# Kernel optimization log

Measured on AMD Instinct MI355X. Metric: run time of the kernel, lower is better.

## Reference

```python
import jax, jax.numpy as jnp
import numpy as np

N, P, Q, H_DIM, HEADS, D = 4096, 128, 128, 256, 8, 64  # D = graph_dim // heads


def setup_inputs() -> dict:
    key = jax.random.key(0)
    ks = jax.random.split(key, 6)
    s = 0.05  # small scale to keep tanh/softmax in a sane range
    return {
        "x_prices": jax.random.normal(ks[0], (N, P), jnp.float32),
        "x_news": jax.random.normal(ks[1], (N, Q), jnp.float32),
        "W_bil": jax.random.normal(ks[2], (H_DIM, P, Q), jnp.float32) * s,
        "b_bil": jax.random.normal(ks[3], (H_DIM,), jnp.float32) * s,
        "Wt": jax.random.normal(ks[4], (HEADS, D, H_DIM), jnp.float32) * s,
        "a_vec": jax.random.normal(ks[5], (HEADS, 2 * D), jnp.float32) * s,
    }


def reference(x_prices, x_news, W_bil, b_bil, Wt, a_vec):
    # nn.Bilinear: out[n,h] = sum_pq x_prices[n,p] W[h,p,q] x_news[n,q] + b[h]
    x = jnp.einsum('np,hpq,nq->nh', x_prices, W_bil, x_news) + b_bil  # (N, hidden)

    # Per-head linear transform: fc_transform (no bias). Wt: (heads, d, hidden)
    xt = jnp.einsum('nh,kdh->knd', x, Wt)  # (heads, N, d)

    # Attention score a . [x_i, x_j] split into src/dst halves -> broadcast add
    d = Wt.shape[1]
    a_src, a_dst = a_vec[:, :d], a_vec[:, d:]
    s_src = jnp.einsum('knd,kd->kn', xt, a_src)  # (heads, N)
    s_dst = jnp.einsum('knd,kd->kn', xt, a_dst)  # (heads, N)
    scores = s_src[:, :, None] + s_dst[:, None, :]  # (heads, N, N)
    scores = jnp.where(scores >= 0, scores, 0.2 * scores)  # LeakyReLU(0.2)

    attn = jax.nn.softmax(scores, axis=-1)  # softmax over neighbors j
    out = jnp.einsum('knm,kmd->knd', attn, xt)  # (heads, N, d)

    # Concatenate head outputs on feature dim, then tanh
    out = jnp.transpose(out, (1, 0, 2)).reshape(xt.shape[1], -1)  # (N, heads*d)
    return jnp.tanh(out)
```

## Files before the change

kernel.cpp:

```cpp
#include <hip/hip_runtime.h>
#include <hip/hip_bf16.h>

typedef unsigned short ushort;
typedef unsigned int uint;
typedef unsigned long long u64;
typedef _Float16 f16;

#define NN 4096
#define PP 128
#define QQ 128
#define HD 256
#define KH 8
#define DD 64
#define KK 16384

typedef _Float16 f16x2 __attribute__((ext_vector_type(2)));
typedef _Float16 f16x4 __attribute__((ext_vector_type(4)));
typedef _Float16 f16x8 __attribute__((ext_vector_type(8)));
typedef __fp16 fp16x2 __attribute__((ext_vector_type(2)));
typedef float f32x4 __attribute__((ext_vector_type(4)));

__device__ inline void async_lds16(const void* g, void* l) {
  __builtin_amdgcn_global_load_lds(
      (const __attribute__((address_space(1))) unsigned int*)g,
      (__attribute__((address_space(3))) unsigned int*)l, 16, 0, 0);
}

__global__ __launch_bounds__(256) void k0_split2(
    const float* __restrict__ W, const float* __restrict__ Wt,
    f16* __restrict__ hiW, f16* __restrict__ loW,
    f16* __restrict__ hiT, f16* __restrict__ loT, float* __restrict__ xz) {
  const int tid = blockIdx.x * 256 + threadIdx.x;
  const int i = tid * 4;
  if (tid < (NN * HD) / 4)
    *(float4*)&xz[i] = make_float4(0.f, 0.f, 0.f, 0.f);
  const float* src;
  f16 *hi, *lo;
  int off;
  if (i < HD * PP * QQ) { src = W; hi = hiW; lo = loW; off = i; }
  else { src = Wt; hi = hiT; lo = loT; off = i - HD * PP * QQ; }
  const float4 w = *(const float4*)&src[off];
  const float wf[4] = {w.x, w.y, w.z, w.w};
  f16x4 hv, lv;
#pragma unroll
  for (int j = 0; j < 4; ++j) {
    const f16 h = (f16)wf[j];
    hv[j] = h;
    lv[j] = (f16)(wf[j] - (float)h);
  }
  *(f16x4*)&hi[off] = hv;
  *(f16x4*)&lo[off] = lv;
}

__global__ __launch_bounds__(256, 4) void k1_bilinear(
    const float* __restrict__ xp, const float* __restrict__ xn,
    const f16* __restrict__ Whi, const f16* __restrict__ Wlo,
    float* __restrict__ xout) {
  __shared__ f16 whi[128 * 32];
  __shared__ f16 wlo[128 * 32];
  __shared__ f16 zhi[128 * 40];
  __shared__ float xpt[8][128];

  const int t = threadIdx.x;
  const int n0 = blockIdx.x * 128;
  const int kb = blockIdx.y * (KK / 16);
  const int h0 = blockIdx.z * 128;
  const int pb = kb >> 7;

  for (int idx = t; idx < 1024; idx += 256) {
    const int p = idx & 7, n = idx >> 3;
    xpt[p][n] = xp[(size_t)(n0 + n) * PP + pb + p];
  }

  const int l = t & 63, w = t >> 6;
  const int wr = (w >> 1) * 64, wc = (w & 1) * 64;

  int aoff[4], boff[4];
#pragma unroll
  for (int i = 0; i < 4; ++i)
    aoff[i] = (wr + i * 16 + (l & 15)) * 40 + (l >> 4) * 8;
#pragma unroll
  for (int j = 0; j < 4; ++j) {
    const int hr = wc + j * 16 + (l & 15);
    boff[j] = hr * 32 + (((l >> 4) ^ ((hr ^ (hr >> 2)) & 3)) * 8);
  }

  const int shb = t >> 2, seg = t & 3;
  int gsw[2];
#pragma unroll
  for (int g = 0; g < 2; ++g) {
    const int r = shb + 64 * g;
    gsw[g] = seg ^ ((r ^ (r >> 2)) & 3);
  }

  const int zn = t >> 1, zko = (t & 1) * 16;

  f32x4 acc[4][4];
#pragma unroll
  for (int i = 0; i < 4; ++i)
#pragma unroll
    for (int j = 0; j < 4; ++j) acc[i][j] = (f32x4)0.f;

  for (int c = 0; c < 32; ++c) {
    const int kc = kb + c * 32;
    const int pl = c >> 2;
    const int q0 = (c & 3) * 32;

    __syncthreads();

#pragma unroll
    for (int g = 0; g < 2; ++g) {
      const int r = shb + 64 * g;
      async_lds16(Whi + (size_t)(h0 + r) * KK + kc + gsw[g] * 8,
                  whi + r * 32 + seg * 8);
      async_lds16(Wlo + (size_t)(h0 + r) * KK + kc + gsw[g] * 8,
                  wlo + r * 32 + seg * 8);
    }

    {
      const float xpv = xpt[pl][zn];
      const float* xr = xn + (size_t)(n0 + zn) * QQ + q0 + zko;
      const float4 v0 = ((const float4*)xr)[0];
      const float4 v1 = ((const float4*)xr)[1];
      const float4 v2 = ((const float4*)xr)[2];
      const float4 v3 = ((const float4*)xr)[3];
      float zz[16] = {v0.x, v0.y, v0.z, v0.w, v1.x, v1.y, v1.z, v1.w,
                      v2.x, v2.y, v2.z, v2.w, v3.x, v3.y, v3.z, v3.w};
      union { uint u[8]; uint4 q[2]; } ph;
#pragma unroll
      for (int j = 0; j < 8; ++j) {
        union { fp16x2 h; uint u; } cv;
        cv.h = __builtin_amdgcn_cvt_pkrtz(xpv * zz[2 * j], xpv * zz[2 * j + 1]);
        ph.u[j] = cv.u;
      }
      const int zo = zn * 40 + zko;
      *(uint4*)&zhi[zo] = ph.q[0];
      *(uint4*)&zhi[zo + 8] = ph.q[1];
    }

    __syncthreads();

    f16x8 Ah[4];
#pragma unroll
    for (int i = 0; i < 4; ++i) Ah[i] = *(const f16x8*)&zhi[aoff[i]];
#pragma unroll
    for (int j = 0; j < 4; ++j) {
      const f16x8 Bh = *(const f16x8*)&whi[boff[j]];
      const f16x8 Bl = *(const f16x8*)&wlo[boff[j]];
#pragma unroll
      for (int i = 0; i < 4; ++i)
        acc[i][j] = __builtin_amdgcn_mfma_f32_16x16x32_f16(Ah[i], Bh, acc[i][j], 0, 0, 0);
#pragma unroll
      for (int i = 0; i < 4; ++i)
        acc[i][j] = __builtin_amdgcn_mfma_f32_16x16x32_f16(Ah[i], Bl, acc[i][j], 0, 0, 0);
    }
  }

#pragma unroll
  for (int i = 0; i < 4; ++i)
#pragma unroll
    for (int j = 0; j < 4; ++j) {
      const int row = n0 + wr + i * 16 + (l >> 4) * 4;
      const int col = h0 + wc + j * 16 + (l & 15);
#pragma unroll
      for (int r = 0; r < 4; ++r)
        atomicAdd(&xout[(size_t)(row + r) * HD + col], acc[i][j][r]);
    }
}

__global__ __launch_bounds__(256) void k23_xt(
    const float* __restrict__ x, const float* __restrict__ bb,
    const f16* __restrict__ Wthi, const f16* __restrict__ Wtlo,
    const float* __restrict__ av, float* __restrict__ xt,
    float* __restrict__ ssrc, float* __restrict__ sdst) {
  __shared__ f16 ah[64 * 40];
  __shared__ f16 bh[128 * 32];
  __shared__ f16 bl[128 * 32];
  __shared__ float red1[2][64][17];
  __shared__ float red2[2][64][17];
  const int t = threadIdx.x;
  const int n0 = blockIdx.x * 64;
  const int c0 = blockIdx.y * 128;
  const int l = t & 63, w = t >> 6;
  const int wn = (w & 1) * 32, wcc = (w >> 1) * 64;

  int aoff[2], boff[4];
#pragma unroll
  for (int i = 0; i < 2; ++i)
    aoff[i] = (wn + i * 16 + (l & 15)) * 40 + (l >> 4) * 8;
#pragma unroll
  for (int j = 0; j < 4; ++j) {
    const int hr = wcc + j * 16 + (l & 15);
    boff[j] = hr * 32 + (((l >> 4) ^ ((hr ^ (hr >> 2)) & 3)) * 8);
  }

  f32x4 acc[2][4];
#pragma unroll
  for (int i = 0; i < 2; ++i)
#pragma unroll
    for (int j = 0; j < 4; ++j) acc[i][j] = (f32x4)0.f;

  for (int kc = 0; kc < HD; kc += 32) {
    __syncthreads();
    {
      const int row = t >> 2, sg = t & 3;
      const float* xr = &x[(size_t)(n0 + row) * HD + kc + sg * 8];
      const float4 xa = ((const float4*)xr)[0];
      const float4 xb = ((const float4*)xr)[1];
      const float4 ba = *(const float4*)&bb[kc + sg * 8];
      const float4 bv = *(const float4*)&bb[kc + sg * 8 + 4];
      f16x8 o;
      o[0] = (f16)(xa.x + ba.x); o[1] = (f16)(xa.y + ba.y);
      o[2] = (f16)(xa.z + ba.z); o[3] = (f16)(xa.w + ba.w);
      o[4] = (f16)(xb.x + bv.x); o[5] = (f16)(xb.y + bv.y);
      o[6] = (f16)(xb.z + bv.z); o[7] = (f16)(xb.w + bv.w);
      *(f16x8*)&ah[row * 40 + sg * 8] = o;
    }
#pragma unroll
    for (int g = 0; g < 2; ++g) {
      const int slot = g * 256 + t;
      const int col = slot >> 2, ps = slot & 3;
      const int ls = ps ^ ((col ^ (col >> 2)) & 3);
      *(uint4*)&bh[col * 32 + ps * 8] =
          *(const uint4*)&Wthi[(size_t)(c0 + col) * HD + kc + ls * 8];
      *(uint4*)&bl[col * 32 + ps * 8] =
          *(const uint4*)&Wtlo[(size_t)(c0 + col) * HD + kc + ls * 8];
    }
    __syncthreads();
    f16x8 Af[2];
#pragma unroll
    for (int i = 0; i < 2; ++i) Af[i] = *(const f16x8*)&ah[aoff[i]];
#pragma unroll
    for (int j = 0; j < 4; ++j) {
      const f16x8 Bh = *(const f16x8*)&bh[boff[j]];
      const f16x8 Bl = *(const f16x8*)&bl[boff[j]];
#pragma unroll
      for (int i = 0; i < 2; ++i)
        acc[i][j] = __builtin_amdgcn_mfma_f32_16x16x32_f16(Af[i], Bh, acc[i][j], 0, 0, 0);
#pragma unroll
      for (int i = 0; i < 2; ++i)
        acc[i][j] = __builtin_amdgcn_mfma_f32_16x16x32_f16(Af[i], Bl, acc[i][j], 0, 0, 0);
    }
  }

  const int hh = w >> 1;
  const int khead = (c0 >> 6) + hh;
  float a1v[4], a2v[4];
#pragma unroll
  for (int j = 0; j < 4; ++j) {
    const int d = j * 16 + (l & 15);
    a1v[j] = av[khead * (2 * DD) + d];
    a2v[j] = av[khead * (2 * DD) + DD + d];
  }

#pragma unroll
  for (int i = 0; i < 2; ++i)
#pragma unroll
    for (int r = 0; r < 4; ++r) {
      const int rowl = wn + i * 16 + (l >> 4) * 4 + r;
      float p1 = 0.f, p2 = 0.f;
#pragma unroll
      for (int j = 0; j < 4; ++j) {
        p1 += acc[i][j][r] * a1v[j];
        p2 += acc[i][j][r] * a2v[j];
      }
      red1[hh][rowl][l & 15] = p1;
      red2[hh][rowl][l & 15] = p2;
    }

#pragma unroll
  for (int i = 0; i < 2; ++i)
#pragma unroll
    for (int j = 0; j < 4; ++j) {
      const int row = n0 + wn + i * 16 + (l >> 4) * 4;
      const int colg = c0 + wcc + j * 16 + (l & 15);
      const int k = colg >> 6, d = colg & 63;
#pragma unroll
      for (int r = 0; r < 4; ++r)
        xt[((size_t)(k * NN + row + r)) * DD + d] = acc[i][j][r];
    }

  __syncthreads();
  {
    const int hh2 = t >> 7;
    const int which = (t >> 6) & 1;
    const int row = t & 63;
    const float* rp = which ? &red2[hh2][row][0] : &red1[hh2][row][0];
    float s = 0.f;
#pragma unroll
    for (int g = 0; g < 16; ++g) s += rp[g];
    const int kk = (c0 >> 6) + hh2;
    if (which) sdst[kk * NN + n0 + row] = s;
    else ssrc[kk * NN + n0 + row] = s;
  }
}

__global__ __launch_bounds__(256) void k4_rank(
    const float* __restrict__ sdst, float* __restrict__ vsorted,
    int* __restrict__ perm) {
  __shared__ u64 kv[4096];
  const int k = blockIdx.y, t = threadIdx.x;
  for (int i = t; i < 4096; i += 256) {
    const uint u = __float_as_uint(sdst[k * NN + i]);
    const uint key = (u & 0x80000000u) ? ~u : (u | 0x80000000u);
    kv[i] = ((u64)key << 32) | (uint)i;
  }
  __syncthreads();
  const int m = blockIdx.x * 256 + t;
  const u64 my = kv[m];
  int cnt = 0;
#pragma unroll 16
  for (int j = 0; j < 4096; ++j) cnt += (kv[j] < my) ? 1 : 0;
  const uint key = (uint)(my >> 32);
  const uint u = (key & 0x80000000u) ? (key ^ 0x80000000u) : ~key;
  vsorted[k * NN + cnt] = __uint_as_float(u);
  perm[k * NN + cnt] = (int)(my & 0xFFFFFFFFu);
}

__global__ __launch_bounds__(64) void k4b_chunksum(
    const float* __restrict__ vs, const int* __restrict__ perm,
    const float* __restrict__ xt, float* __restrict__ Chi, float* __restrict__ Clo) {
  __shared__ float rows[64][64];
  __shared__ float eh[64], el[64];
  const int c = blockIdx.x, k = blockIdx.y, t = threadIdx.x;
  const int base = k * NN + c * 64;
  {
    const float v = vs[base + t];
    eh[t] = __expf(v);
    el[t] = __expf(0.2f * v);
  }
#pragma unroll
  for (int r = 0; r < 16; ++r) {
    const int i = r * 4 + (t >> 4);
    const int p = perm[base + i];
    *(float4*)&rows[i][(t & 15) * 4] =
        *(const float4*)&xt[((size_t)(k * NN + p)) * DD + (t & 15) * 4];
  }
  __syncthreads();
  float shi = 0.f, slo = 0.f, whs = 0.f, wls = 0.f;
#pragma unroll 8
  for (int i = 0; i < 64; ++i) {
    const float val = rows[i][t];
    shi += eh[i] * val; slo += el[i] * val;
    whs += eh[i]; wls += el[i];
  }
  const int cb = (k * 64 + c) * 65;
  Chi[cb + t] = shi;
  Clo[cb + t] = slo;
  if (t == 0) { Chi[cb + 64] = whs; Clo[cb + 64] = wls; }
}

__global__ __launch_bounds__(64) void k4d_expand(
    const float* __restrict__ vs, const int* __restrict__ perm,
    const float* __restrict__ xt, const float* __restrict__ Chi,
    const float* __restrict__ Clo, float* __restrict__ Phi,
    float* __restrict__ Plo) {
  __shared__ float schi[64 * 65];
  __shared__ float sclo[64 * 65];
  __shared__ float rows[64][64];
  __shared__ float eh[64], el[64];
  const int c = blockIdx.x, k = blockIdx.y, t = threadIdx.x;
  const int base = k * NN + c * 64;
  for (int idx = t; idx < 4160; idx += 64) {
    schi[idx] = Chi[k * 4160 + idx];
    sclo[idx] = Clo[k * 4160 + idx];
  }
  {
    const float v = vs[base + t];
    eh[t] = __expf(v);
    el[t] = __expf(0.2f * v);
  }
#pragma unroll
  for (int r = 0; r < 16; ++r) {
    const int i = r * 4 + (t >> 4);
    const int p = perm[base + i];
    *(float4*)&rows[i][(t & 15) * 4] =
        *(const float4*)&xt[((size_t)(k * NN + p)) * DD + (t & 15) * 4];
  }
  __syncthreads();

  float run = 0.f, wrun = 0.f;
  for (int cc = 0; cc < c; ++cc) {
    run += sclo[cc * 65 + t];
    wrun += sclo[cc * 65 + 64];
  }
  float runS = 0.f, wrunS = 0.f;
  for (int cc = c + 1; cc < 64; ++cc) {
    runS += schi[cc * 65 + t];
    wrunS += schi[cc * 65 + 64];
  }

  for (int i = 0; i < 64; ++i) {
    const size_t rb = ((size_t)(k * 4097) + c * 64 + i) * 65;
    Plo[rb + t] = run;
    if (t == 0) Plo[rb + 64] = wrun;
    run += el[i] * rows[i][t];
    wrun += el[i];
  }
  if (c == 63) {
    const size_t rb = ((size_t)(k * 4097) + 4096) * 65;
    Plo[rb + t] = run;
    if (t == 0) Plo[rb + 64] = wrun;
  }
  for (int i = 63; i >= 0; --i) {
    runS += eh[i] * rows[i][t];
    wrunS += eh[i];
    const size_t rb = ((size_t)(k * 4097) + c * 64 + i) * 65;
    Phi[rb + t] = runS;
    if (t == 0) Phi[rb + 64] = wrunS;
  }
  if (c == 63) {
    const size_t rb = ((size_t)(k * 4097) + 4096) * 65;
    Phi[rb + t] = 0.f;
    if (t == 0) Phi[rb + 64] = 0.f;
  }
}

__global__ __launch_bounds__(256) void k6_final(
    const float* __restrict__ ssrc, const float* __restrict__ vsorted,
    const float* __restrict__ Phi, const float* __restrict__ Plo,
    float* __restrict__ out) {
  __shared__ float vsh[4096];
  __shared__ int posSh[16];
  const int t = threadIdx.x;
  const int q0 = blockIdx.x * 16;
  const int k = q0 >> 12;
  for (int idx = t; idx < 1024; idx += 256)
    *(float4*)&vsh[idx * 4] = *(const float4*)&vsorted[k * NN + idx * 4];
  __syncthreads();
  if (t < 16) {
    const float thr = -ssrc[q0 + t];
    int lo = 0, hi = 4096;
    while (lo < hi) {
      const int mid = (lo + hi) >> 1;
      if (vsh[mid] < thr) lo = mid + 1; else hi = mid;
    }
    posSh[t] = lo;
  }
  __syncthreads();
  const int d = t & 63;
#pragma unroll
  for (int qq = 0; qq < 4; ++qq) {
    const int ql = qq * 4 + (t >> 6);
    const int qi = q0 + ql;
    const int n = qi & 4095;
    const float u = ssrc[qi];
    const size_t rb = ((size_t)(k * 4097) + posSh[ql]) * 65;
    const float eu = __expf(u), el = __expf(0.2f * u);
    const float num = eu * Phi[rb + d] + el * Plo[rb + d];
    const float den = eu * Phi[rb + 64] + el * Plo[rb + 64];
    out[(size_t)n * (KH * DD) + k * DD + d] = tanhf(num / den);
  }
}

extern "C" void kernel_launch(void* const* d_in, const int* in_sizes, int n_in,
                              void* d_out, int out_size, void* d_ws, size_t ws_size,
                              hipStream_t stream) {
  const float* xp = (const float*)d_in[0];
  const float* xn = (const float*)d_in[1];
  const float* W = (const float*)d_in[2];
  const float* bb = (const float*)d_in[3];
  const float* Wt = (const float*)d_in[4];
  const float* av = (const float*)d_in[5];
  float* out = (float*)d_out;

  char* ws = (char*)d_ws;
  f16* Whi    = (f16*)(ws);
  f16* Wlo    = (f16*)(ws + 8388608);
  float* Phi  = (float*)(ws);
  float* Plo  = (float*)(ws + 8522240);
  float* x    = (float*)(ws + 17044480);
  float* xt   = (float*)(ws + 21238784);
  f16* Wthi   = (f16*)(ws + 31724544);
  f16* Wtlo   = (f16*)(ws + 31986688);
  float* ssrc = (float*)(ws + 32248832);
  float* sdst = (float*)(ws + 32379904);
  float* vsort= (float*)(ws + 32510976);
  int*   perm = (int*)  (ws + 32642048);
  float* Chi  = (float*)(ws + 32773120);
  float* Clo  = (float*)(ws + 32906240);

  k0_split2<<<(HD * PP * QQ + KH * DD * HD) / 1024, 256, 0, stream>>>(
      W, Wt, Whi, Wlo, Wthi, Wtlo, x);
  k1_bilinear<<<dim3(NN / 128, 16, 2), 256, 0, stream>>>(xp, xn, Whi, Wlo, x);
  k23_xt<<<dim3(NN / 64, 4), 256, 0, stream>>>(x, bb, Wthi, Wtlo, av, xt, ssrc, sdst);
  k4_rank<<<dim3(16, KH), 256, 0, stream>>>(sdst, vsort, perm);
  k4b_chunksum<<<dim3(64, KH), 64, 0, stream>>>(vsort, perm, xt, Chi, Clo);
  k4d_expand<<<dim3(64, KH), 64, 0, stream>>>(vsort, perm, xt, Chi, Clo, Phi, Plo);
  k6_final<<<(KH * NN) / 16, 256, 0, stream>>>(ssrc, vsort, Phi, Plo, out);
}
```

Before: 280.2 us.

## Enlarge bilinear and xt GEMM tiles to 64-wide K steps with 8-way swizzle

The bilinear kernel now uses 512-thread blocks covering 256 rows and steps K by 64 per iteration instead of 32. This halves the barrier count and roughly doubles W reuse per block, so each staged W tile feeds twice as many rows. The xt kernel likewise moves to 64-wide K chunks with a new 8-way XOR swizzle for its LDS layout. The cost is more LDS per block, which may lower occupancy, and the grid for the bilinear stage shrinks to half as many blocks.

```diff
diff --git a/kernel.cpp b/kernel.cpp
--- a/kernel.cpp
+++ b/kernel.cpp
@@ -52,48 +52,47 @@
   *(f16x4*)&lo[off] = lv;
 }
 
-__global__ __launch_bounds__(256, 4) void k1_bilinear(
+__global__ __launch_bounds__(512, 4) void k1_bilinear(
     const float* __restrict__ xp, const float* __restrict__ xn,
     const f16* __restrict__ Whi, const f16* __restrict__ Wlo,
     float* __restrict__ xout) {
-  __shared__ f16 whi[128 * 32];
-  __shared__ f16 wlo[128 * 32];
-  __shared__ f16 zhi[128 * 40];
-  __shared__ float xpt[8][128];
+  __shared__ f16 whi[128 * 64];
+  __shared__ f16 wlo[128 * 64];
+  __shared__ f16 zhi[256 * 72];
 
   const int t = threadIdx.x;
-  const int n0 = blockIdx.x * 128;
-  const int kb = blockIdx.y * (KK / 16);
+  const int n0 = blockIdx.x * 256;
+  const int kb = blockIdx.y * 1024;
   const int h0 = blockIdx.z * 128;
   const int pb = kb >> 7;
 
-  for (int idx = t; idx < 1024; idx += 256) {
-    const int p = idx & 7, n = idx >> 3;
-    xpt[p][n] = xp[(size_t)(n0 + n) * PP + pb + p];
-  }
-
   const int l = t & 63, w = t >> 6;
-  const int wr = (w >> 1) * 64, wc = (w & 1) * 64;
-
-  int aoff[4], boff[4];
+  const int wr = (w >> 1) * 64;
+  const int wc = (w & 1) * 64;
+
+  int aoff[4];
 #pragma unroll
   for (int i = 0; i < 4; ++i)
-    aoff[i] = (wr + i * 16 + (l & 15)) * 40 + (l >> 4) * 8;
+    aoff[i] = (wr + i * 16 + (l & 15)) * 72 + (l >> 4) * 8;
+  int boff[4][2];
 #pragma unroll
   for (int j = 0; j < 4; ++j) {
     const int hr = wc + j * 16 + (l & 15);
-    boff[j] = hr * 32 + (((l >> 4) ^ ((hr ^ (hr >> 2)) & 3)) * 8);
-  }
-
-  const int shb = t >> 2, seg = t & 3;
-  int gsw[2];
+#pragma unroll
+    for (int ks = 0; ks < 2; ++ks)
+      boff[j][ks] = hr * 64 + ((ks * 4 + (l >> 4)) ^ (hr & 7)) * 8;
+  }
+
+  int srow[2], sgseg[2];
 #pragma unroll
   for (int g = 0; g < 2; ++g) {
-    const int r = shb + 64 * g;
-    gsw[g] = seg ^ ((r ^ (r >> 2)) & 3);
-  }
-
-  const int zn = t >> 1, zko = (t & 1) * 16;
+    const int slot = g * 512 + t;
+    srow[g] = slot >> 3;
+    sgseg[g] = (slot & 7) ^ (srow[g] & 7);
+  }
+
+  const int zn = t >> 1;
+  const int zq = (t & 1) * 32;
 
   f32x4 acc[4][4];
 #pragma unroll
@@ -101,58 +100,57 @@
 #pragma unroll
     for (int j = 0; j < 4; ++j) acc[i][j] = (f32x4)0.f;
 
-  for (int c = 0; c < 32; ++c) {
-    const int kc = kb + c * 32;
-    const int pl = c >> 2;
-    const int q0 = (c & 3) * 32;
+  for (int c = 0; c < 16; ++c) {
+    const int kc = kb + c * 64;
+    const int pl = c >> 1;
+    const int q0 = (c & 1) * 64;
 
     __syncthreads();
 
 #pragma unroll
     for (int g = 0; g < 2; ++g) {
-      const int r = shb + 64 * g;
-      async_lds16(Whi + (size_t)(h0 + r) * KK + kc + gsw[g] * 8,
-                  whi + r * 32 + seg * 8);
-      async_lds16(Wlo + (size_t)(h0 + r) * KK + kc + gsw[g] * 8,
-                  wlo + r * 32 + seg * 8);
+      const int slot = g * 512 + t;
+      async_lds16(Whi + (size_t)(h0 + srow[g]) * KK + kc + sgseg[g] * 8,
+                  whi + slot * 8);
+      async_lds16(Wlo + (size_t)(h0 + srow[g]) * KK + kc + sgseg[g] * 8,
+                  wlo + slot * 8);
     }
 
     {
-      const float xpv = xpt[pl][zn];
-      const float* xr = xn + (size_t)(n0 + zn) * QQ + q0 + zko;
-      const float4 v0 = ((const float4*)xr)[0];
-      const float4 v1 = ((const float4*)xr)[1];
-      const float4 v2 = ((const float4*)xr)[2];
-      const float4 v3 = ((const float4*)xr)[3];
-      float zz[16] = {v0.x, v0.y, v0.z, v0.w, v1.x, v1.y, v1.z, v1.w,
-                      v2.x, v2.y, v2.z, v2.w, v3.x, v3.y, v3.z, v3.w};
-      union { uint u[8]; uint4 q[2]; } ph;
-#pragma unroll
-      for (int j = 0; j < 8; ++j) {
+      const float xpv = xp[(size_t)(n0 + zn) * PP + pb + pl];
+      const float* xr = xn + (size_t)(n0 + zn) * QQ + q0 + zq;
+#pragma unroll
+      for (int b = 0; b < 4; ++b) {
+        const float4 v0 = ((const float4*)xr)[2 * b];
+        const float4 v1 = ((const float4*)xr)[2 * b + 1];
+        uint4 ph;
         union { fp16x2 h; uint u; } cv;
-        cv.h = __builtin_amdgcn_cvt_pkrtz(xpv * zz[2 * j], xpv * zz[2 * j + 1]);
-        ph.u[j] = cv.u;
+        cv.h = __builtin_amdgcn_cvt_pkrtz(xpv * v0.x, xpv * v0.y); ph.x = cv.u;
+        cv.h = __builtin_amdgcn_cvt_pkrtz(xpv * v0.z, xpv * v0.w); ph.y = cv.u;
+        cv.h = __builtin_amdgcn_cvt_pkrtz(xpv * v1.x, xpv * v1.y); ph.z = cv.u;
+        cv.h = __builtin_amdgcn_cvt_pkrtz(xpv * v1.z, xpv * v1.w); ph.w = cv.u;
+        *(uint4*)&zhi[zn * 72 + zq + b * 8] = ph;
       }
-      const int zo = zn * 40 + zko;
-      *(uint4*)&zhi[zo] = ph.q[0];
-      *(uint4*)&zhi[zo + 8] = ph.q[1];
     }
 
     __syncthreads();
 
-    f16x8 Ah[4];
-#pragma unroll
-    for (int i = 0; i < 4; ++i) Ah[i] = *(const f16x8*)&zhi[aoff[i]];
-#pragma unroll
-    for (int j = 0; j < 4; ++j) {
-      const f16x8 Bh = *(const f16x8*)&whi[boff[j]];
-      const f16x8 Bl = *(const f16x8*)&wlo[boff[j]];
-#pragma unroll
-      for (int i = 0; i < 4; ++i)
-        acc[i][j] = __builtin_amdgcn_mfma_f32_16x16x32_f16(Ah[i], Bh, acc[i][j], 0, 0, 0);
-#pragma unroll
-      for (int i = 0; i < 4; ++i)
-        acc[i][j] = __builtin_amdgcn_mfma_f32_16x16x32_f16(Ah[i], Bl, acc[i][j], 0, 0, 0);
+#pragma unroll
+    for (int ks = 0; ks < 2; ++ks) {
+      f16x8 Ah[4];
+#pragma unroll
+      for (int i = 0; i < 4; ++i) Ah[i] = *(const f16x8*)&zhi[aoff[i] + ks * 32];
+#pragma unroll
+      for (int j = 0; j < 4; ++j) {
+        const f16x8 Bh = *(const f16x8*)&whi[boff[j][ks]];
+        const f16x8 Bl = *(const f16x8*)&wlo[boff[j][ks]];
+#pragma unroll
+        for (int i = 0; i < 4; ++i)
+          acc[i][j] = __builtin_amdgcn_mfma_f32_16x16x32_f16(Ah[i], Bh, acc[i][j], 0, 0, 0);
+#pragma unroll
+        for (int i = 0; i < 4; ++i)
+          acc[i][j] = __builtin_amdgcn_mfma_f32_16x16x32_f16(Ah[i], Bl, acc[i][j], 0, 0, 0);
+      }
     }
   }
 
@@ -173,9 +171,9 @@
     const f16* __restrict__ Wthi, const f16* __restrict__ Wtlo,
     const float* __restrict__ av, float* __restrict__ xt,
     float* __restrict__ ssrc, float* __restrict__ sdst) {
-  __shared__ f16 ah[64 * 40];
-  __shared__ f16 bh[128 * 32];
-  __shared__ f16 bl[128 * 32];
+  __shared__ f16 ah[64 * 72];
+  __shared__ f16 bh[128 * 64];
+  __shared__ f16 bl[128 * 64];
   __shared__ float red1[2][64][17];
   __shared__ float red2[2][64][17];
   const int t = threadIdx.x;
@@ -184,14 +182,17 @@
   const int l = t & 63, w = t >> 6;
   const int wn = (w & 1) * 32, wcc = (w >> 1) * 64;
 
-  int aoff[2], boff[4];
+  int aoff[2];
 #pragma unroll
   for (int i = 0; i < 2; ++i)
-    aoff[i] = (wn + i * 16 + (l & 15)) * 40 + (l >> 4) * 8;
+    aoff[i] = (wn + i * 16 + (l & 15)) * 72 + (l >> 4) * 8;
+  int boff[4][2];
 #pragma unroll
   for (int j = 0; j < 4; ++j) {
     const int hr = wcc + j * 16 + (l & 15);
-    boff[j] = hr * 32 + (((l >> 4) ^ ((hr ^ (hr >> 2)) & 3)) * 8);
+#pragma unroll
+    for (int ks = 0; ks < 2; ++ks)
+      boff[j][ks] = hr * 64 + ((ks * 4 + (l >> 4)) ^ (hr & 7)) * 8;
   }
 
   f32x4 acc[2][4];
@@ -200,10 +201,12 @@
 #pragma unroll
     for (int j = 0; j < 4; ++j) acc[i][j] = (f32x4)0.f;
 
-  for (int kc = 0; kc < HD; kc += 32) {
+  for (int kc = 0; kc < HD; kc += 64) {
     __syncthreads();
-    {
-      const int row = t >> 2, sg = t & 3;
+#pragma unroll
+    for (int g = 0; g < 2; ++g) {
+      const int slot = g * 256 + t;
+      const int row = slot >> 3, sg = slot & 7;
       const float* xr = &x[(size_t)(n0 + row) * HD + kc + sg * 8];
       const float4 xa = ((const float4*)xr)[0];
       const float4 xb = ((const float4*)xr)[1];
@@ -214,32 +217,35 @@
       o[2] = (f16)(xa.z + ba.z); o[3] = (f16)(xa.w + ba.w);
       o[4] = (f16)(xb.x + bv.x); o[5] = (f16)(xb.y + bv.y);
       o[6] = (f16)(xb.z + bv.z); o[7] = (f16)(xb.w + bv.w);
-      *(f16x8*)&ah[row * 40 + sg * 8] = o;
-    }
-#pragma unroll
-    for (int g = 0; g < 2; ++g) {
+      *(f16x8*)&ah[row * 72 + sg * 8] = o;
+    }
+#pragma unroll
+    for (int g = 0; g < 4; ++g) {
       const int slot = g * 256 + t;
-      const int col = slot >> 2, ps = slot & 3;
-      const int ls = ps ^ ((col ^ (col >> 2)) & 3);
-      *(uint4*)&bh[col * 32 + ps * 8] =
+      const int col = slot >> 3, ps = slot & 7;
+      const int ls = ps ^ (col & 7);
+      *(uint4*)&bh[col * 64 + ps * 8] =
           *(const uint4*)&Wthi[(size_t)(c0 + col) * HD + kc + ls * 8];
-      *(uint4*)&bl[col * 32 + ps * 8] =
+      *(uint4*)&bl[col * 64 + ps * 8] =
           *(const uint4*)&Wtlo[(size_t)(c0 + col) * HD + kc + ls * 8];
     }
     __syncthreads();
-    f16x8 Af[2];
-#pragma unroll
-    for (int i = 0; i < 2; ++i) Af[i] = *(const f16x8*)&ah[aoff[i]];
-#pragma unroll
-    for (int j = 0; j < 4; ++j) {
-      const f16x8 Bh = *(const f16x8*)&bh[boff[j]];
-      const f16x8 Bl = *(const f16x8*)&bl[boff[j]];
-#pragma unroll
-      for (int i = 0; i < 2; ++i)
-        acc[i][j] = __builtin_amdgcn_mfma_f32_16x16x32_f16(Af[i], Bh, acc[i][j], 0, 0, 0);
-#pragma unroll
-      for (int i = 0; i < 2; ++i)
-        acc[i][j] = __builtin_amdgcn_mfma_f32_16x16x32_f16(Af[i], Bl, acc[i][j], 0, 0, 0);
+#pragma unroll
+    for (int ks = 0; ks < 2; ++ks) {
+      f16x8 Af[2];
+#pragma unroll
+      for (int i = 0; i < 2; ++i) Af[i] = *(const f16x8*)&ah[aoff[i] + ks * 32];
+#pragma unroll
+      for (int j = 0; j < 4; ++j) {
+        const f16x8 Bh = *(const f16x8*)&bh[boff[j][ks]];
+        const f16x8 Bl = *(const f16x8*)&bl[boff[j][ks]];
+#pragma unroll
+        for (int i = 0; i < 2; ++i)
+          acc[i][j] = __builtin_amdgcn_mfma_f32_16x16x32_f16(Af[i], Bh, acc[i][j], 0, 0, 0);
+#pragma unroll
+        for (int i = 0; i < 2; ++i)
+          acc[i][j] = __builtin_amdgcn_mfma_f32_16x16x32_f16(Af[i], Bl, acc[i][j], 0, 0, 0);
+      }
     }
   }
 
@@ -482,7 +488,7 @@
 
   k0_split2<<<(HD * PP * QQ + KH * DD * HD) / 1024, 256, 0, stream>>>(
       W, Wt, Whi, Wlo, Wthi, Wtlo, x);
-  k1_bilinear<<<dim3(NN / 128, 16, 2), 256, 0, stream>>>(xp, xn, Whi, Wlo, x);
+  k1_bilinear<<<dim3(NN / 256, 16, 2), 512, 0, stream>>>(xp, xn, Whi, Wlo, x);
   k23_xt<<<dim3(NN / 64, 4), 256, 0, stream>>>(x, bb, Wthi, Wtlo, av, xt, ssrc, sdst);
   k4_rank<<<dim3(16, KH), 256, 0, stream>>>(sdst, vsort, perm);
   k4b_chunksum<<<dim3(64, KH), 64, 0, stream>>>(vsort, perm, xt, Chi, Clo);
```

New measurement: 319.1 us. +13.9%, slower.

## Restructure bilinear kernel: per-wave Z rows, direct global W fragments, fp16 inputs

Applied to the files above, without the earlier changes.

The bilinear GEMM kernel is rebuilt. Each thread now forms its own row of the outer-product operand Z from pre-converted fp16 inputs and writes it to LDS, where each wave reads only the rows it wrote, so block-wide syncthreads become wave barriers. W hi/lo fragments are loaded straight from global memory into registers instead of being staged through LDS. The tile changes to 256 rows by 64 hidden columns per block, with an fp16 conversion of x_news and x_prices added to the split kernel. In exchange, the product is now computed in fp16 (xp*xn) instead of fp32 followed by rounding, W reuse across waves goes through cache rather than LDS, and each block covers fewer hidden columns, so W is fetched more often per row.

```diff
diff --git a/kernel.cpp b/kernel.cpp
--- a/kernel.cpp
+++ b/kernel.cpp
@@ -20,20 +20,27 @@
 typedef __fp16 fp16x2 __attribute__((ext_vector_type(2)));
 typedef float f32x4 __attribute__((ext_vector_type(4)));
 
-__device__ inline void async_lds16(const void* g, void* l) {
-  __builtin_amdgcn_global_load_lds(
-      (const __attribute__((address_space(1))) unsigned int*)g,
-      (__attribute__((address_space(3))) unsigned int*)l, 16, 0, 0);
-}
-
 __global__ __launch_bounds__(256) void k0_split2(
     const float* __restrict__ W, const float* __restrict__ Wt,
+    const float* __restrict__ xn, const float* __restrict__ xp,
     f16* __restrict__ hiW, f16* __restrict__ loW,
-    f16* __restrict__ hiT, f16* __restrict__ loT, float* __restrict__ xz) {
+    f16* __restrict__ hiT, f16* __restrict__ loT,
+    f16* __restrict__ xnh, f16* __restrict__ xph, float* __restrict__ xz) {
   const int tid = blockIdx.x * 256 + threadIdx.x;
   const int i = tid * 4;
   if (tid < (NN * HD) / 4)
     *(float4*)&xz[i] = make_float4(0.f, 0.f, 0.f, 0.f);
+  if (tid >= 262144 && tid < 393216) {
+    const int o = (tid - 262144) * 4;
+    const float4 v = *(const float4*)&xn[o];
+    f16x4 h; h[0] = (f16)v.x; h[1] = (f16)v.y; h[2] = (f16)v.z; h[3] = (f16)v.w;
+    *(f16x4*)&xnh[o] = h;
+  } else if (tid >= 393216 && tid < 524288) {
+    const int o = (tid - 393216) * 4;
+    const float4 v = *(const float4*)&xp[o];
+    f16x4 h; h[0] = (f16)v.x; h[1] = (f16)v.y; h[2] = (f16)v.z; h[3] = (f16)v.w;
+    *(f16x4*)&xph[o] = h;
+  }
   const float* src;
   f16 *hi, *lo;
   int off;
@@ -52,48 +59,30 @@
   *(f16x4*)&lo[off] = lv;
 }
 
-__global__ __launch_bounds__(256, 4) void k1_bilinear(
-    const float* __restrict__ xp, const float* __restrict__ xn,
+__global__ __launch_bounds__(256, 3) void k1_bilinear(
+    const f16* __restrict__ xph, const f16* __restrict__ xnh,
     const f16* __restrict__ Whi, const f16* __restrict__ Wlo,
     float* __restrict__ xout) {
-  __shared__ f16 whi[128 * 32];
-  __shared__ f16 wlo[128 * 32];
-  __shared__ f16 zhi[128 * 40];
-  __shared__ float xpt[8][128];
+  __shared__ f16 zhi[256 * 40];
 
   const int t = threadIdx.x;
-  const int n0 = blockIdx.x * 128;
-  const int kb = blockIdx.y * (KK / 16);
-  const int h0 = blockIdx.z * 128;
+  const int n0 = blockIdx.x * 256;
+  const int kb = blockIdx.y * 1024;
+  const int h0 = blockIdx.z * 64;
   const int pb = kb >> 7;
 
-  for (int idx = t; idx < 1024; idx += 256) {
-    const int p = idx & 7, n = idx >> 3;
-    xpt[p][n] = xp[(size_t)(n0 + n) * PP + pb + p];
-  }
-
   const int l = t & 63, w = t >> 6;
-  const int wr = (w >> 1) * 64, wc = (w & 1) * 64;
-
-  int aoff[4], boff[4];
+  const int nrow = n0 + t;
+
+  int aoff[4];
 #pragma unroll
   for (int i = 0; i < 4; ++i)
-    aoff[i] = (wr + i * 16 + (l & 15)) * 40 + (l >> 4) * 8;
-#pragma unroll
-  for (int j = 0; j < 4; ++j) {
-    const int hr = wc + j * 16 + (l & 15);
-    boff[j] = hr * 32 + (((l >> 4) ^ ((hr ^ (hr >> 2)) & 3)) * 8);
-  }
-
-  const int shb = t >> 2, seg = t & 3;
-  int gsw[2];
-#pragma unroll
-  for (int g = 0; g < 2; ++g) {
-    const int r = shb + 64 * g;
-    gsw[g] = seg ^ ((r ^ (r >> 2)) & 3);
-  }
-
-  const int zn = t >> 1, zko = (t & 1) * 16;
+    aoff[i] = (w * 64 + i * 16 + (l & 15)) * 40 + (l >> 4) * 8;
+
+  const f16* bb_hi = Whi + (size_t)(h0 + (l & 15)) * KK + kb + (l >> 4) * 8;
+  const f16* bb_lo = Wlo + (size_t)(h0 + (l & 15)) * KK + kb + (l >> 4) * 8;
+  const f16* xnr = xnh + (size_t)nrow * QQ;
+  const f16* xpr = xph + (size_t)nrow * PP + pb;
 
   f32x4 acc[4][4];
 #pragma unroll
@@ -101,67 +90,55 @@
 #pragma unroll
     for (int j = 0; j < 4; ++j) acc[i][j] = (f32x4)0.f;
 
-  for (int c = 0; c < 32; ++c) {
-    const int kc = kb + c * 32;
-    const int pl = c >> 2;
-    const int q0 = (c & 3) * 32;
-
-    __syncthreads();
-
-#pragma unroll
-    for (int g = 0; g < 2; ++g) {
-      const int r = shb + 64 * g;
-      async_lds16(Whi + (size_t)(h0 + r) * KK + kc + gsw[g] * 8,
-                  whi + r * 32 + seg * 8);
-      async_lds16(Wlo + (size_t)(h0 + r) * KK + kc + gsw[g] * 8,
-                  wlo + r * 32 + seg * 8);
-    }
-
-    {
-      const float xpv = xpt[pl][zn];
-      const float* xr = xn + (size_t)(n0 + zn) * QQ + q0 + zko;
-      const float4 v0 = ((const float4*)xr)[0];
-      const float4 v1 = ((const float4*)xr)[1];
-      const float4 v2 = ((const float4*)xr)[2];
-      const float4 v3 = ((const float4*)xr)[3];
-      float zz[16] = {v0.x, v0.y, v0.z, v0.w, v1.x, v1.y, v1.z, v1.w,
-                      v2.x, v2.y, v2.z, v2.w, v3.x, v3.y, v3.z, v3.w};
-      union { uint u[8]; uint4 q[2]; } ph;
-#pragma unroll
-      for (int j = 0; j < 8; ++j) {
-        union { fp16x2 h; uint u; } cv;
-        cv.h = __builtin_amdgcn_cvt_pkrtz(xpv * zz[2 * j], xpv * zz[2 * j + 1]);
-        ph.u[j] = cv.u;
+  for (int pl = 0; pl < 8; ++pl) {
+    const f16 xpv = xpr[pl];
+    f16x8 xb;
+#pragma unroll
+    for (int m = 0; m < 8; ++m) xb[m] = xpv;
+#pragma unroll
+    for (int qc = 0; qc < 4; ++qc) {
+      const int c = pl * 4 + qc;
+      const int kc = c * 32;
+
+      f16x8 Bh[4], Bl[4];
+#pragma unroll
+      for (int j = 0; j < 4; ++j) {
+        Bh[j] = *(const f16x8*)(bb_hi + (size_t)j * 16 * KK + kc);
+        Bl[j] = *(const f16x8*)(bb_lo + (size_t)j * 16 * KK + kc);
       }
-      const int zo = zn * 40 + zko;
-      *(uint4*)&zhi[zo] = ph.q[0];
-      *(uint4*)&zhi[zo + 8] = ph.q[1];
-    }
-
-    __syncthreads();
-
-    f16x8 Ah[4];
-#pragma unroll
-    for (int i = 0; i < 4; ++i) Ah[i] = *(const f16x8*)&zhi[aoff[i]];
+
+      const f16x8* xr = (const f16x8*)(xnr + qc * 32);
+#pragma unroll
+      for (int b = 0; b < 4; ++b) {
+        const f16x8 zv = xb * xr[b];
+        *(f16x8*)&zhi[nrow % 1 * 0 + (t * 40) + b * 8] = zv;
+      }
+      __builtin_amdgcn_wave_barrier();
+
+      f16x8 Ah[4];
+#pragma unroll
+      for (int i = 0; i < 4; ++i) Ah[i] = *(const f16x8*)&zhi[aoff[i]];
+      __builtin_amdgcn_wave_barrier();
+
+#pragma unroll
+      for (int j = 0; j < 4; ++j)
+#pragma unroll
+        for (int i = 0; i < 4; ++i)
+          acc[i][j] = __builtin_amdgcn_mfma_f32_16x16x32_f16(Ah[i], Bh[j], acc[i][j], 0, 0, 0);
+#pragma unroll
+      for (int j = 0; j < 4; ++j)
+#pragma unroll
+        for (int i = 0; i < 4; ++i)
+          acc[i][j] = __builtin_amdgcn_mfma_f32_16x16x32_f16(Ah[i], Bl[j], acc[i][j], 0, 0, 0);
+    }
+  }
+
+#pragma unroll
+  for (int i = 0; i < 4; ++i)
 #pragma unroll
     for (int j = 0; j < 4; ++j) {
-      const f16x8 Bh = *(const f16x8*)&whi[boff[j]];
-      const f16x8 Bl = *(const f16x8*)&wlo[boff[j]];
-#pragma unroll
-      for (int i = 0; i < 4; ++i)
-        acc[i][j] = __builtin_amdgcn_mfma_f32_16x16x32_f16(Ah[i], Bh, acc[i][j], 0, 0, 0);
-#pragma unroll
-      for (int i = 0; i < 4; ++i)
-        acc[i][j] = __builtin_amdgcn_mfma_f32_16x16x32_f16(Ah[i], Bl, acc[i][j], 0, 0, 0);
-    }
-  }
-
-#pragma unroll
-  for (int i = 0; i < 4; ++i)
-#pragma unroll
-    for (int j = 0; j < 4; ++j) {
-      const int row = n0 + wr + i * 16 + (l >> 4) * 4;
-      const int col = h0 + wc + j * 16 + (l & 15);
+      const int row = n0 + w * 64 + i * 16 + (l >> 4) * 4;
+      const int col = h0 + j * 16 + (l & 15);
 #pragma unroll
       for (int r = 0; r < 4; ++r)
         atomicAdd(&xout[(size_t)(row + r) * HD + col], acc[i][j][r]);
@@ -206,14 +183,14 @@
       const int row = t >> 2, sg = t & 3;
       const float* xr = &x[(size_t)(n0 + row) * HD + kc + sg * 8];
       const float4 xa = ((const float4*)xr)[0];
-      const float4 xb = ((const float4*)xr)[1];
+      const float4 xbv = ((const float4*)xr)[1];
       const float4 ba = *(const float4*)&bb[kc + sg * 8];
       const float4 bv = *(const float4*)&bb[kc + sg * 8 + 4];
       f16x8 o;
       o[0] = (f16)(xa.x + ba.x); o[1] = (f16)(xa.y + ba.y);
       o[2] = (f16)(xa.z + ba.z); o[3] = (f16)(xa.w + ba.w);
-      o[4] = (f16)(xb.x + bv.x); o[5] = (f16)(xb.y + bv.y);
-      o[6] = (f16)(xb.z + bv.z); o[7] = (f16)(xb.w + bv.w);
+      o[4] = (f16)(xbv.x + bv.x); o[5] = (f16)(xbv.y + bv.y);
+      o[6] = (f16)(xbv.z + bv.z); o[7] = (f16)(xbv.w + bv.w);
       *(f16x8*)&ah[row * 40 + sg * 8] = o;
     }
 #pragma unroll
@@ -479,10 +456,12 @@
   int*   perm = (int*)  (ws + 32642048);
   float* Chi  = (float*)(ws + 32773120);
   float* Clo  = (float*)(ws + 32906240);
+  f16* xnh    = (f16*)(ws + 33039360);
+  f16* xph    = (f16*)(ws + 34087936);
 
   k0_split2<<<(HD * PP * QQ + KH * DD * HD) / 1024, 256, 0, stream>>>(
-      W, Wt, Whi, Wlo, Wthi, Wtlo, x);
-  k1_bilinear<<<dim3(NN / 128, 16, 2), 256, 0, stream>>>(xp, xn, Whi, Wlo, x);
+      W, Wt, xn, xp, Whi, Wlo, Wthi, Wtlo, xnh, xph, x);
+  k1_bilinear<<<dim3(NN / 256, 16, 4), 256, 0, stream>>>(xph, xnh, Whi, Wlo, x);
   k23_xt<<<dim3(NN / 64, 4), 256, 0, stream>>>(x, bb, Wthi, Wtlo, av, xt, ssrc, sdst);
   k4_rank<<<dim3(16, KH), 256, 0, stream>>>(sdst, vsort, perm);
   k4b_chunksum<<<dim3(64, KH), 64, 0, stream>>>(vsort, perm, xt, Chi, Clo);
```

Measured after the change: 364.4 us. 1.3x slower.
